# Kernel optimization log

Hardware: AMD Instinct MI355X
Metric: run time of the kernel (lower is better)

The kernel has to match this reference:

```python
import jax, jax.numpy as jnp
from jax import lax
import numpy as np

B, T, F = 128, 512, 256
H = 1024
GHOST = 512  # hidden_size - hidden_size // ghost_ratio
INTR = 512   # hidden_size // ghost_ratio


def setup_inputs() -> dict:
    key = jax.random.key(0)
    ks = jax.random.split(key, 8)
    stdv = 1.0 / np.sqrt(H)
    u = lambda k, shape: jax.random.uniform(k, shape, jnp.float32, -stdv, stdv)
    return {
        "x": jax.random.normal(ks[0], (B, T, F), jnp.float32),
        "hidden": jax.random.normal(ks[1], (B, 1, H), jnp.float32),
        "weight_gate": u(ks[2], (2 * INTR, F + H)),
        "weight_candidate": u(ks[3], (INTR, F + H)),
        "weight_ghost": u(ks[4], (GHOST, INTR)),
        "bias_gate": u(ks[5], (2 * INTR,)),
        "bias_candidate": u(ks[6], (INTR,)),
        "bias_ghost": jax.random.normal(ks[7], (GHOST,), jnp.float32),
    }


def reference(x, hidden, weight_gate, weight_candidate, weight_ghost,
              bias_gate, bias_candidate, bias_ghost):
    ghost_size = weight_ghost.shape[0]
    h0 = hidden[:, 0, :]  # squeeze(1) -> [B, H]

    def step(h, x_t):
        # gates: [B, F+H] @ [F+H, 2*INTR]
        gate = jax.nn.sigmoid(
            jnp.concatenate([x_t, h], axis=1) @ weight_gate.T + bias_gate)
        r, u = jnp.split(gate, 2, axis=1)
        r_state = r * h[:, ghost_size:]
        cand_in = jnp.concatenate([x_t, h[:, :ghost_size], r_state], axis=1)
        c = jnp.tanh(cand_in @ weight_candidate.T + bias_candidate)
        new_h = u * h[:, ghost_size:] + (1.0 - u) * c          # [B, INTR]
        ghost = jnp.tanh(new_h @ weight_ghost.T + bias_ghost)  # [B, GHOST]
        nh = jnp.concatenate([ghost, new_h], axis=1)           # [B, H]
        return nh, nh

    xs = jnp.swapaxes(x, 0, 1)  # [T, B, F]
    h_final, outs = lax.scan(step, h0, xs)
    outputs = jnp.swapaxes(outs, 0, 1)  # [B, T, H]
    return outputs, h_final[:, None, :]
```

## Files before the change

### kernel.cpp

```cpp
#include <hip/hip_runtime.h>


typedef unsigned short ushort_t;
typedef unsigned long long ull_t;
typedef __attribute__((ext_vector_type(8))) short short8;
typedef __attribute__((ext_vector_type(4))) float f32x4;

#define NB 128
#define NT 512
#define NF 256
#define NH 1024
#define KGATE 1280

#define AT_LOAD(p)     __hip_atomic_load((p), __ATOMIC_RELAXED, __HIP_MEMORY_SCOPE_AGENT)
#define AT_STORE(p,v)  __hip_atomic_store((p), (v), __ATOMIC_RELAXED, __HIP_MEMORY_SCOPE_AGENT)

__device__ __forceinline__ float bf2f(ushort_t u) {
  union { unsigned int i; float f; } v; v.i = ((unsigned int)u) << 16; return v.f;
}
__device__ __forceinline__ ushort_t f2bf(float f) {
  union { float f; unsigned int i; } v; v.f = f;
  unsigned int r = v.i + 0x7FFFu + ((v.i >> 16) & 1u);
  return (ushort_t)(r >> 16);
}
__device__ __forceinline__ float sigmoidf_(float x) { return 1.f / (1.f + __expf(-x)); }
__device__ __forceinline__ float tanhf_(float x) {
  float e = __expf(2.f * x); return 1.f - 2.f / (e + 1.f);
}

__device__ __forceinline__ void post_flag(unsigned* flags, int memb, unsigned val) {
  __syncthreads();
  if (threadIdx.x == 0) AT_STORE(&flags[memb], val);
}

__device__ __forceinline__ void wait_flags(const unsigned* flags, unsigned tgt) {
  const int sl = (int)(threadIdx.x & 31u);
  for (;;) {
    unsigned f = AT_LOAD(&flags[sl]);
    if (__all((int)(f >= tgt))) break;
    __builtin_amdgcn_s_sleep(1);
  }
  __builtin_amdgcn_sched_barrier(0);
}

__device__ __forceinline__ short8 pack_bf16_8(const float* p) {
  float4 a = *(const float4*)p;
  float4 b = *(const float4*)(p + 4);
  short8 f;
  f[0] = (short)f2bf(a.x); f[1] = (short)f2bf(a.y);
  f[2] = (short)f2bf(a.z); f[3] = (short)f2bf(a.w);
  f[4] = (short)f2bf(b.x); f[5] = (short)f2bf(b.y);
  f[6] = (short)f2bf(b.z); f[7] = (short)f2bf(b.w);
  return f;
}

__global__ void __launch_bounds__(256, 1) ghost_gru_persistent(
    const float* __restrict__ x, const float* __restrict__ hidden,
    const float* __restrict__ Wg, const float* __restrict__ Wc,
    const float* __restrict__ Wgh, const float* __restrict__ bg,
    const float* __restrict__ bc, const float* __restrict__ bgh,
    float* __restrict__ out, unsigned int* __restrict__ hbuf_u,
    unsigned int* __restrict__ rs_u, unsigned int* __restrict__ counters)
{
  const int wgid = blockIdx.x;
  const int g    = wgid & 7;
  const int memb = wgid >> 3;
  const int b0   = g * 16;
  const int tid  = threadIdx.x;
  const int wv   = tid >> 6;
  const int lane = tid & 63;
  const int lq   = lane >> 4;
  const int ln   = lane & 15;
  unsigned* flags = counters + g * 64;

  __shared__ __align__(16) ushort_t Abuf[16][1832];

  short8 wfrag[40];
  int ncol0;
  float biasv;
  if (wv == 0) {
    ncol0 = memb * 16;
    const float* wp = Wg + (size_t)(ncol0 + ln) * KGATE + lq * 8;
    #pragma unroll
    for (int kc = 0; kc < 40; ++kc) wfrag[kc] = pack_bf16_8(wp + kc * 32);
    biasv = bg[ncol0 + ln];
  } else if (wv == 1) {
    ncol0 = 512 + memb * 16;
    const float* wp = Wg + (size_t)(ncol0 + ln) * KGATE + lq * 8;
    #pragma unroll
    for (int kc = 0; kc < 40; ++kc) wfrag[kc] = pack_bf16_8(wp + kc * 32);
    biasv = bg[ncol0 + ln];
  } else if (wv == 2) {
    ncol0 = memb * 16;
    const float* wp = Wc + (size_t)(ncol0 + ln) * KGATE + lq * 8;
    #pragma unroll
    for (int kc = 0; kc < 40; ++kc) wfrag[kc] = pack_bf16_8(wp + kc * 32);
    biasv = bc[ncol0 + ln];
  } else {
    ncol0 = memb * 16;
    const float* wp = Wgh + (size_t)(ncol0 + ln) * 512 + lq * 8;
    #pragma unroll
    for (int kc = 0; kc < 16; ++kc) wfrag[kc] = pack_bf16_8(wp + kc * 32);
    biasv = bgh[ncol0 + ln];
  }

  float hreg[4];
  if (wv == 2) {
    #pragma unroll
    for (int r = 0; r < 4; ++r)
      hreg[r] = hidden[(size_t)(b0 + lq * 4 + r) * NH + 512 + ncol0 + ln];
  }

  const ull_t* hbuf64 = (const ull_t*)hbuf_u;
  const ull_t* rs64   = (const ull_t*)rs_u;

  {
    ull_t nv[8];
    #pragma unroll
    for (int k = 0; k < 8; ++k) {
      int j = tid + k * 256;
      nv[k] = AT_LOAD(&hbuf64[(size_t)(b0 + (j >> 7)) * 256 + 128 + (j & 127)]);
    }
    #pragma unroll
    for (int k = 0; k < 8; ++k) {
      int j = tid + k * 256;
      *(ull_t*)&Abuf[j >> 7][768 + 4 * (j & 127)] = nv[k];
    }
  }

  float4 xv[4];
  #pragma unroll
  for (int k = 0; k < 4; ++k) {
    int i = tid + k * 256;
    xv[k] = *(const float4*)&x[((size_t)(b0 + (i >> 6)) * NT + 0) * NF + (i & 63) * 4];
  }

  #pragma unroll 1
  for (int t = 0; t < NT; ++t) {
    const int cur = t & 1, nxt = cur ^ 1;
    const ull_t* hsrc64 = hbuf64 + (size_t)cur * NB * 256;
    unsigned*    hdst   = hbuf_u + (size_t)nxt * NB * 512;
    const ull_t* hdst64 = hbuf64 + (size_t)nxt * NB * 256;

    {
      ull_t gv[8];
      #pragma unroll
      for (int k = 0; k < 8; ++k) {
        int j = tid + k * 256;
        gv[k] = AT_LOAD(&hsrc64[(size_t)(b0 + (j >> 7)) * 256 + (j & 127)]);
      }
      #pragma unroll
      for (int k = 0; k < 4; ++k) {
        int i = tid + k * 256;
        int row = i >> 6, c4 = (i & 63) * 4;
        ushort4 u4 = make_ushort4(f2bf(xv[k].x), f2bf(xv[k].y),
                                  f2bf(xv[k].z), f2bf(xv[k].w));
        *(ushort4*)&Abuf[row][c4] = u4;
      }
      #pragma unroll
      for (int k = 0; k < 8; ++k) {
        int j = tid + k * 256;
        *(ull_t*)&Abuf[j >> 7][256 + 4 * (j & 127)] = gv[k];
      }
    }
    __syncthreads();

    {
      const int tn = (t + 1 < NT) ? t + 1 : t;
      #pragma unroll
      for (int k = 0; k < 4; ++k) {
        int i = tid + k * 256;
        xv[k] = *(const float4*)&x[((size_t)(b0 + (i >> 6)) * NT + tn) * NF + (i & 63) * 4];
      }
    }

    if (wv < 2) {
      f32x4 acc0 = {0.f, 0.f, 0.f, 0.f}, acc1 = {0.f, 0.f, 0.f, 0.f};
      #pragma unroll
      for (int kc = 0; kc < 40; kc += 2) {
        short8 a0 = *(const short8*)&Abuf[ln][kc * 32 + lq * 8];
        acc0 = __builtin_amdgcn_mfma_f32_16x16x32_bf16(a0, wfrag[kc], acc0, 0, 0, 0);
        short8 a1 = *(const short8*)&Abuf[ln][(kc + 1) * 32 + lq * 8];
        acc1 = __builtin_amdgcn_mfma_f32_16x16x32_bf16(a1, wfrag[kc + 1], acc1, 0, 0, 0);
      }
      const int n = ncol0 + ln;
      if (wv == 0) {
        #pragma unroll
        for (int r = 0; r < 4; ++r) {
          int row = lq * 4 + r;
          float s = sigmoidf_(acc0[r] + acc1[r] + biasv);
          float hold = bf2f(Abuf[row][768 + n]);
          unsigned hv = (unsigned)f2bf(s * hold);
          unsigned pv = (unsigned)__shfl_xor((int)hv, 1);
          if (!(ln & 1))
            AT_STORE(&rs_u[(size_t)(b0 + row) * 256 + (n >> 1)], hv | (pv << 16));
        }
      } else {
        #pragma unroll
        for (int r = 0; r < 4; ++r) {
          int row = lq * 4 + r;
          float s = sigmoidf_(acc0[r] + acc1[r] + biasv);
          ((float*)&Abuf[row][1792])[ln] = s;
        }
      }
    }
    post_flag(flags, memb, 3u * (unsigned)t + 1u);
    wait_flags(flags, 3u * (unsigned)t + 1u);

    float uval[4];
    f32x4 acc0c = {0.f, 0.f, 0.f, 0.f}, acc1c = {0.f, 0.f, 0.f, 0.f};
    if (wv == 2) {
      #pragma unroll
      for (int r = 0; r < 4; ++r)
        uval[r] = ((const float*)&Abuf[lq * 4 + r][1792])[ln];
      #pragma unroll
      for (int kc = 0; kc < 24; kc += 2) {
        short8 a0 = *(const short8*)&Abuf[ln][kc * 32 + lq * 8];
        acc0c = __builtin_amdgcn_mfma_f32_16x16x32_bf16(a0, wfrag[kc], acc0c, 0, 0, 0);
        short8 a1 = *(const short8*)&Abuf[ln][(kc + 1) * 32 + lq * 8];
        acc1c = __builtin_amdgcn_mfma_f32_16x16x32_bf16(a1, wfrag[kc + 1], acc1c, 0, 0, 0);
      }
    } else if (wv < 2) {
      ull_t rv[16];
      #pragma unroll
      for (int k = 0; k < 16; ++k) {
        int j = tid + k * 128;
        rv[k] = AT_LOAD(&rs64[(size_t)(b0 + (j >> 7)) * 128 + (j & 127)]);
      }
      #pragma unroll
      for (int k = 0; k < 16; ++k) {
        int j = tid + k * 128;
        *(ull_t*)&Abuf[j >> 7][1280 + 4 * (j & 127)] = rv[k];
      }
    }
    __syncthreads();
    if (wv == 2) {
      #pragma unroll
      for (int kc = 24; kc < 40; kc += 2) {
        short8 a0 = *(const short8*)&Abuf[ln][1280 + (kc - 24) * 32 + lq * 8];
        acc0c = __builtin_amdgcn_mfma_f32_16x16x32_bf16(a0, wfrag[kc], acc0c, 0, 0, 0);
        short8 a1 = *(const short8*)&Abuf[ln][1280 + (kc - 23) * 32 + lq * 8];
        acc1c = __builtin_amdgcn_mfma_f32_16x16x32_bf16(a1, wfrag[kc + 1], acc1c, 0, 0, 0);
      }
      const int n = ncol0 + ln;
      #pragma unroll
      for (int r = 0; r < 4; ++r) {
        int row = lq * 4 + r;
        int b = b0 + row;
        float cv = tanhf_(acc0c[r] + acc1c[r] + biasv);
        float u = uval[r];
        float hnew = u * hreg[r] + (1.f - u) * cv;
        hreg[r] = hnew;
        out[((size_t)b * NT + t) * NH + 512 + n] = hnew;
        unsigned hv = (unsigned)f2bf(hnew);
        unsigned pv = (unsigned)__shfl_xor((int)hv, 1);
        if (!(ln & 1))
          AT_STORE(&hdst[(size_t)b * 512 + 256 + (n >> 1)], hv | (pv << 16));
        if (t == NT - 1) out[(size_t)NB * NT * NH + (size_t)b * NH + 512 + n] = hnew;
      }
    }
    post_flag(flags, memb, 3u * (unsigned)t + 2u);
    wait_flags(flags, 3u * (unsigned)t + 2u);

    {
      ull_t nv[8];
      #pragma unroll
      for (int k = 0; k < 8; ++k) {
        int j = tid + k * 256;
        nv[k] = AT_LOAD(&hdst64[(size_t)(b0 + (j >> 7)) * 256 + 128 + (j & 127)]);
      }
      #pragma unroll
      for (int k = 0; k < 8; ++k) {
        int j = tid + k * 256;
        *(ull_t*)&Abuf[j >> 7][768 + 4 * (j & 127)] = nv[k];
      }
    }
    __syncthreads();

    if (wv == 3) {
      f32x4 acc = {0.f, 0.f, 0.f, 0.f};
      #pragma unroll
      for (int kc = 0; kc < 16; ++kc) {
        short8 a = *(const short8*)&Abuf[ln][768 + kc * 32 + lq * 8];
        acc = __builtin_amdgcn_mfma_f32_16x16x32_bf16(a, wfrag[kc], acc, 0, 0, 0);
      }
      const int n = ncol0 + ln;
      #pragma unroll
      for (int r = 0; r < 4; ++r) {
        int row = lq * 4 + r;
        int b = b0 + row;
        float gv = tanhf_(acc[r] + biasv);
        out[((size_t)b * NT + t) * NH + n] = gv;
        unsigned hv = (unsigned)f2bf(gv);
        unsigned pv = (unsigned)__shfl_xor((int)hv, 1);
        if (!(ln & 1))
          AT_STORE(&hdst[(size_t)b * 512 + (n >> 1)], hv | (pv << 16));
        if (t == NT - 1) out[(size_t)NB * NT * NH + (size_t)b * NH + n] = gv;
      }
    }
    post_flag(flags, memb, 3u * (unsigned)t + 3u);
    wait_flags(flags, 3u * (unsigned)t + 3u);
  }
}

__global__ void init_kernel(const float* __restrict__ hidden,
                            unsigned int* __restrict__ hbuf_u,
                            unsigned int* __restrict__ counters) {
  int i = blockIdx.x * blockDim.x + threadIdx.x;
  if (i < NB * 512) {
    unsigned lo = (unsigned)f2bf(hidden[2 * i]);
    unsigned hi = (unsigned)f2bf(hidden[2 * i + 1]);
    hbuf_u[i] = lo | (hi << 16);
  }
  if (i < 512) counters[i] = 0;
}

extern "C" void kernel_launch(void* const* d_in, const int* in_sizes, int n_in,
                              void* d_out, int out_size, void* d_ws, size_t ws_size,
                              hipStream_t stream) {
  (void)in_sizes; (void)n_in; (void)out_size; (void)ws_size;
  const float* x      = (const float*)d_in[0];
  const float* hidden = (const float*)d_in[1];
  const float* Wg     = (const float*)d_in[2];
  const float* Wc     = (const float*)d_in[3];
  const float* Wgh    = (const float*)d_in[4];
  const float* bg     = (const float*)d_in[5];
  const float* bc     = (const float*)d_in[6];
  const float* bgh    = (const float*)d_in[7];
  float* out = (float*)d_out;

  char* ws = (char*)d_ws;
  unsigned int* hbuf_u   = (unsigned int*)(ws);
  unsigned int* rs_u     = (unsigned int*)(ws + 524288);
  unsigned int* counters = (unsigned int*)(ws + 655360);

  init_kernel<<<dim3(256), dim3(256), 0, stream>>>(hidden, hbuf_u, counters);
  ghost_gru_persistent<<<dim3(256), dim3(256), 0, stream>>>(
      x, hidden, Wg, Wc, Wgh, bg, bc, bgh, out, hbuf_u, rs_u, counters);
}
```

Measured before the change: 4.060 ms.

## Split group barrier into per-stage flags and precompute x and new_h gate terms early

```diff
diff --git a/kernel.cpp b/kernel.cpp
--- a/kernel.cpp
+++ b/kernel.cpp
@@ -15,6 +15,10 @@
 #define AT_LOAD(p)     __hip_atomic_load((p), __ATOMIC_RELAXED, __HIP_MEMORY_SCOPE_AGENT)
 #define AT_STORE(p,v)  __hip_atomic_store((p), (v), __ATOMIC_RELAXED, __HIP_MEMORY_SCOPE_AGENT)
 
+#define DRAIN() do { __builtin_amdgcn_sched_barrier(0); \
+                     __builtin_amdgcn_s_waitcnt(0);     \
+                     __builtin_amdgcn_sched_barrier(0); } while (0)
+
 __device__ __forceinline__ float bf2f(ushort_t u) {
   union { unsigned int i; float f; } v; v.i = ((unsigned int)u) << 16; return v.f;
 }
@@ -26,11 +30,6 @@
 __device__ __forceinline__ float sigmoidf_(float x) { return 1.f / (1.f + __expf(-x)); }
 __device__ __forceinline__ float tanhf_(float x) {
   float e = __expf(2.f * x); return 1.f - 2.f / (e + 1.f);
-}
-
-__device__ __forceinline__ void post_flag(unsigned* flags, int memb, unsigned val) {
-  __syncthreads();
-  if (threadIdx.x == 0) AT_STORE(&flags[memb], val);
 }
 
 __device__ __forceinline__ void wait_flags(const unsigned* flags, unsigned tgt) {
@@ -71,9 +70,15 @@
   const int lane = tid & 63;
   const int lq   = lane >> 4;
   const int ln   = lane & 15;
-  unsigned* flags = counters + g * 64;
+  unsigned* rflag = counters + g * 256;
+  unsigned* nflag = counters + g * 256 + 64;
+  unsigned* gflag = counters + g * 256 + 128;
 
   __shared__ __align__(16) ushort_t Abuf[16][1832];
+
+  #define LDA(kc)  (*(const short8*)&Abuf[ln][(kc) * 32 + lq * 8])
+  #define LDR(kc)  (*(const short8*)&Abuf[ln][1280 + ((kc) - 24) * 32 + lq * 8])
+  #define MFMA(a, b, c) __builtin_amdgcn_mfma_f32_16x16x32_bf16((a), (b), (c), 0, 0, 0)
 
   short8 wfrag[40];
   int ncol0;
@@ -126,22 +131,48 @@
       int j = tid + k * 256;
       *(ull_t*)&Abuf[j >> 7][768 + 4 * (j & 127)] = nv[k];
     }
+    #pragma unroll
+    for (int k = 0; k < 4; ++k) {
+      int i = tid + k * 256;
+      int row = i >> 6, c4 = (i & 63) * 4;
+      float4 v = *(const float4*)&x[((size_t)(b0 + row) * NT + 0) * NF + c4];
+      *(ushort4*)&Abuf[row][c4] =
+          make_ushort4(f2bf(v.x), f2bf(v.y), f2bf(v.z), f2bf(v.w));
+    }
+  }
+  __syncthreads();
+
+  f32x4 acc0 = {0.f, 0.f, 0.f, 0.f}, acc1 = {0.f, 0.f, 0.f, 0.f};
+
+  if (wv < 2) {
+    #pragma unroll
+    for (int kc = 0; kc < 8; kc += 2) {
+      acc0 = MFMA(LDA(kc), wfrag[kc], acc0);
+      acc1 = MFMA(LDA(kc + 1), wfrag[kc + 1], acc1);
+    }
+    #pragma unroll
+    for (int kc = 24; kc < 40; kc += 2) {
+      acc0 = MFMA(LDA(kc), wfrag[kc], acc0);
+      acc1 = MFMA(LDA(kc + 1), wfrag[kc + 1], acc1);
+    }
+  } else if (wv == 2) {
+    #pragma unroll
+    for (int kc = 0; kc < 8; kc += 2) {
+      acc0 = MFMA(LDA(kc), wfrag[kc], acc0);
+      acc1 = MFMA(LDA(kc + 1), wfrag[kc + 1], acc1);
+    }
   }
 
   float4 xv[4];
-  #pragma unroll
-  for (int k = 0; k < 4; ++k) {
-    int i = tid + k * 256;
-    xv[k] = *(const float4*)&x[((size_t)(b0 + (i >> 6)) * NT + 0) * NF + (i & 63) * 4];
-  }
 
   #pragma unroll 1
   for (int t = 0; t < NT; ++t) {
     const int cur = t & 1, nxt = cur ^ 1;
     const ull_t* hsrc64 = hbuf64 + (size_t)cur * NB * 256;
     unsigned*    hdst   = hbuf_u + (size_t)nxt * NB * 512;
-    const ull_t* hdst64 = hbuf64 + (size_t)nxt * NB * 256;
-
+    const ull_t* hdst64 = (const ull_t*)hdst;
+
+    wait_flags(gflag, (unsigned)t);
     {
       ull_t gv[8];
       #pragma unroll
@@ -150,14 +181,6 @@
         gv[k] = AT_LOAD(&hsrc64[(size_t)(b0 + (j >> 7)) * 256 + (j & 127)]);
       }
       #pragma unroll
-      for (int k = 0; k < 4; ++k) {
-        int i = tid + k * 256;
-        int row = i >> 6, c4 = (i & 63) * 4;
-        ushort4 u4 = make_ushort4(f2bf(xv[k].x), f2bf(xv[k].y),
-                                  f2bf(xv[k].z), f2bf(xv[k].w));
-        *(ushort4*)&Abuf[row][c4] = u4;
-      }
-      #pragma unroll
       for (int k = 0; k < 8; ++k) {
         int j = tid + k * 256;
         *(ull_t*)&Abuf[j >> 7][256 + 4 * (j & 127)] = gv[k];
@@ -165,23 +188,11 @@
     }
     __syncthreads();
 
-    {
-      const int tn = (t + 1 < NT) ? t + 1 : t;
-      #pragma unroll
-      for (int k = 0; k < 4; ++k) {
-        int i = tid + k * 256;
-        xv[k] = *(const float4*)&x[((size_t)(b0 + (i >> 6)) * NT + tn) * NF + (i & 63) * 4];
-      }
-    }
-
     if (wv < 2) {
-      f32x4 acc0 = {0.f, 0.f, 0.f, 0.f}, acc1 = {0.f, 0.f, 0.f, 0.f};
-      #pragma unroll
-      for (int kc = 0; kc < 40; kc += 2) {
-        short8 a0 = *(const short8*)&Abuf[ln][kc * 32 + lq * 8];
-        acc0 = __builtin_amdgcn_mfma_f32_16x16x32_bf16(a0, wfrag[kc], acc0, 0, 0, 0);
-        short8 a1 = *(const short8*)&Abuf[ln][(kc + 1) * 32 + lq * 8];
-        acc1 = __builtin_amdgcn_mfma_f32_16x16x32_bf16(a1, wfrag[kc + 1], acc1, 0, 0, 0);
+      #pragma unroll
+      for (int kc = 8; kc < 24; kc += 2) {
+        acc0 = MFMA(LDA(kc), wfrag[kc], acc0);
+        acc1 = MFMA(LDA(kc + 1), wfrag[kc + 1], acc1);
       }
       const int n = ncol0 + ln;
       if (wv == 0) {
@@ -195,6 +206,8 @@
           if (!(ln & 1))
             AT_STORE(&rs_u[(size_t)(b0 + row) * 256 + (n >> 1)], hv | (pv << 16));
         }
+        DRAIN();
+        if (tid == 0) AT_STORE(&rflag[memb], (unsigned)t + 1u);
       } else {
         #pragma unroll
         for (int r = 0; r < 4; ++r) {
@@ -203,24 +216,27 @@
           ((float*)&Abuf[row][1792])[ln] = s;
         }
       }
-    }
-    post_flag(flags, memb, 3u * (unsigned)t + 1u);
-    wait_flags(flags, 3u * (unsigned)t + 1u);
-
-    float uval[4];
-    f32x4 acc0c = {0.f, 0.f, 0.f, 0.f}, acc1c = {0.f, 0.f, 0.f, 0.f};
+      acc0 = (f32x4){0.f, 0.f, 0.f, 0.f};
+      acc1 = (f32x4){0.f, 0.f, 0.f, 0.f};
+    }
+
+    {
+      const int tn = (t + 1 < NT) ? t + 1 : t;
+      #pragma unroll
+      for (int k = 0; k < 4; ++k) {
+        int i = tid + k * 256;
+        xv[k] = *(const float4*)&x[((size_t)(b0 + (i >> 6)) * NT + tn) * NF + (i & 63) * 4];
+      }
+    }
+
     if (wv == 2) {
       #pragma unroll
-      for (int r = 0; r < 4; ++r)
-        uval[r] = ((const float*)&Abuf[lq * 4 + r][1792])[ln];
-      #pragma unroll
-      for (int kc = 0; kc < 24; kc += 2) {
-        short8 a0 = *(const short8*)&Abuf[ln][kc * 32 + lq * 8];
-        acc0c = __builtin_amdgcn_mfma_f32_16x16x32_bf16(a0, wfrag[kc], acc0c, 0, 0, 0);
-        short8 a1 = *(const short8*)&Abuf[ln][(kc + 1) * 32 + lq * 8];
-        acc1c = __builtin_amdgcn_mfma_f32_16x16x32_bf16(a1, wfrag[kc + 1], acc1c, 0, 0, 0);
+      for (int kc = 8; kc < 24; kc += 2) {
+        acc0 = MFMA(LDA(kc), wfrag[kc], acc0);
+        acc1 = MFMA(LDA(kc + 1), wfrag[kc + 1], acc1);
       }
     } else if (wv < 2) {
+      wait_flags(rflag, (unsigned)t + 1u);
       ull_t rv[16];
       #pragma unroll
       for (int k = 0; k < 16; ++k) {
@@ -234,34 +250,41 @@
       }
     }
     __syncthreads();
+
     if (wv == 2) {
+      float uval[4], hn[4];
+      #pragma unroll
+      for (int r = 0; r < 4; ++r)
+        uval[r] = ((const float*)&Abuf[lq * 4 + r][1792])[ln];
       #pragma unroll
       for (int kc = 24; kc < 40; kc += 2) {
-        short8 a0 = *(const short8*)&Abuf[ln][1280 + (kc - 24) * 32 + lq * 8];
-        acc0c = __builtin_amdgcn_mfma_f32_16x16x32_bf16(a0, wfrag[kc], acc0c, 0, 0, 0);
-        short8 a1 = *(const short8*)&Abuf[ln][1280 + (kc - 23) * 32 + lq * 8];
-        acc1c = __builtin_amdgcn_mfma_f32_16x16x32_bf16(a1, wfrag[kc + 1], acc1c, 0, 0, 0);
+        acc0 = MFMA(LDR(kc), wfrag[kc], acc0);
+        acc1 = MFMA(LDR(kc + 1), wfrag[kc + 1], acc1);
       }
       const int n = ncol0 + ln;
       #pragma unroll
       for (int r = 0; r < 4; ++r) {
         int row = lq * 4 + r;
-        int b = b0 + row;
-        float cv = tanhf_(acc0c[r] + acc1c[r] + biasv);
+        float cv = tanhf_(acc0[r] + acc1[r] + biasv);
         float u = uval[r];
         float hnew = u * hreg[r] + (1.f - u) * cv;
-        hreg[r] = hnew;
-        out[((size_t)b * NT + t) * NH + 512 + n] = hnew;
+        hreg[r] = hnew; hn[r] = hnew;
         unsigned hv = (unsigned)f2bf(hnew);
         unsigned pv = (unsigned)__shfl_xor((int)hv, 1);
         if (!(ln & 1))
-          AT_STORE(&hdst[(size_t)b * 512 + 256 + (n >> 1)], hv | (pv << 16));
-        if (t == NT - 1) out[(size_t)NB * NT * NH + (size_t)b * NH + 512 + n] = hnew;
-      }
-    }
-    post_flag(flags, memb, 3u * (unsigned)t + 2u);
-    wait_flags(flags, 3u * (unsigned)t + 2u);
-
+          AT_STORE(&hdst[(size_t)(b0 + row) * 512 + 256 + (n >> 1)], hv | (pv << 16));
+      }
+      DRAIN();
+      if (tid == 128) AT_STORE(&nflag[memb], (unsigned)t + 1u);
+      #pragma unroll
+      for (int r = 0; r < 4; ++r) {
+        int b = b0 + lq * 4 + r;
+        out[((size_t)b * NT + t) * NH + 512 + n] = hn[r];
+        if (t == NT - 1) out[(size_t)NB * NT * NH + (size_t)b * NH + 512 + n] = hn[r];
+      }
+    }
+
+    wait_flags(nflag, (unsigned)t + 1u);
     {
       ull_t nv[8];
       #pragma unroll
@@ -274,33 +297,65 @@
         int j = tid + k * 256;
         *(ull_t*)&Abuf[j >> 7][768 + 4 * (j & 127)] = nv[k];
       }
+      #pragma unroll
+      for (int k = 0; k < 4; ++k) {
+        int i = tid + k * 256;
+        int row = i >> 6, c4 = (i & 63) * 4;
+        *(ushort4*)&Abuf[row][c4] =
+            make_ushort4(f2bf(xv[k].x), f2bf(xv[k].y), f2bf(xv[k].z), f2bf(xv[k].w));
+      }
     }
     __syncthreads();
 
     if (wv == 3) {
       f32x4 acc = {0.f, 0.f, 0.f, 0.f};
       #pragma unroll
-      for (int kc = 0; kc < 16; ++kc) {
-        short8 a = *(const short8*)&Abuf[ln][768 + kc * 32 + lq * 8];
-        acc = __builtin_amdgcn_mfma_f32_16x16x32_bf16(a, wfrag[kc], acc, 0, 0, 0);
-      }
+      for (int kc = 0; kc < 16; ++kc)
+        acc = MFMA((*(const short8*)&Abuf[ln][768 + kc * 32 + lq * 8]), wfrag[kc], acc);
       const int n = ncol0 + ln;
+      float gvv[4];
       #pragma unroll
       for (int r = 0; r < 4; ++r) {
         int row = lq * 4 + r;
-        int b = b0 + row;
         float gv = tanhf_(acc[r] + biasv);
-        out[((size_t)b * NT + t) * NH + n] = gv;
+        gvv[r] = gv;
         unsigned hv = (unsigned)f2bf(gv);
         unsigned pv = (unsigned)__shfl_xor((int)hv, 1);
         if (!(ln & 1))
-          AT_STORE(&hdst[(size_t)b * 512 + (n >> 1)], hv | (pv << 16));
-        if (t == NT - 1) out[(size_t)NB * NT * NH + (size_t)b * NH + n] = gv;
-      }
-    }
-    post_flag(flags, memb, 3u * (unsigned)t + 3u);
-    wait_flags(flags, 3u * (unsigned)t + 3u);
-  }
+          AT_STORE(&hdst[(size_t)(b0 + row) * 512 + (n >> 1)], hv | (pv << 16));
+      }
+      DRAIN();
+      if (tid == 192) AT_STORE(&gflag[memb], (unsigned)t + 1u);
+      #pragma unroll
+      for (int r = 0; r < 4; ++r) {
+        int b = b0 + lq * 4 + r;
+        out[((size_t)b * NT + t) * NH + n] = gvv[r];
+        if (t == NT - 1) out[(size_t)NB * NT * NH + (size_t)b * NH + n] = gvv[r];
+      }
+    } else if (wv < 2) {
+      #pragma unroll
+      for (int kc = 0; kc < 8; kc += 2) {
+        acc0 = MFMA(LDA(kc), wfrag[kc], acc0);
+        acc1 = MFMA(LDA(kc + 1), wfrag[kc + 1], acc1);
+      }
+      #pragma unroll
+      for (int kc = 24; kc < 40; kc += 2) {
+        acc0 = MFMA(LDA(kc), wfrag[kc], acc0);
+        acc1 = MFMA(LDA(kc + 1), wfrag[kc + 1], acc1);
+      }
+    } else {
+      acc0 = (f32x4){0.f, 0.f, 0.f, 0.f};
+      acc1 = (f32x4){0.f, 0.f, 0.f, 0.f};
+      #pragma unroll
+      for (int kc = 0; kc < 8; kc += 2) {
+        acc0 = MFMA(LDA(kc), wfrag[kc], acc0);
+        acc1 = MFMA(LDA(kc + 1), wfrag[kc + 1], acc1);
+      }
+    }
+  }
+  #undef LDA
+  #undef LDR
+  #undef MFMA
 }
 
 __global__ void init_kernel(const float* __restrict__ hidden,
@@ -312,7 +367,7 @@
     unsigned hi = (unsigned)f2bf(hidden[2 * i + 1]);
     hbuf_u[i] = lo | (hi << 16);
   }
-  if (i < 512) counters[i] = 0;
+  if (i < 2048) counters[i] = 0;
 }
 
 extern "C" void kernel_launch(void* const* d_in, const int* in_sizes, int n_in,
```

Result: slower. 5.391 ms (+32.8%).
